# Performance work log

Hardware: AMD Instinct MI355X
Metric: run time of the kernel (lower is better)

The kernel has to match this reference:

```python
import jax, jax.numpy as jnp
import numpy as np

N_NODES = 100_000
N_EDGES = 1_600_000  # random edges; self-loops appended (add_self_edges_networkx)
IN_FEATS = 64
N_HIDDEN = 64
N_CLASSES = 40


def setup_inputs() -> dict:
    key = jax.random.key(0)
    ks = jax.random.split(key, 10)
    features = jax.random.normal(ks[0], (N_NODES, IN_FEATS), jnp.float32)
    self_loops = jnp.arange(N_NODES, dtype=jnp.int32)
    src = jnp.concatenate([jax.random.randint(ks[1], (N_EDGES,), 0, N_NODES, jnp.int32), self_loops])
    dst = jnp.concatenate([jax.random.randint(ks[2], (N_EDGES,), 0, N_NODES, jnp.int32), self_loops])
    labels = jax.random.randint(ks[3], (N_NODES,), 0, N_CLASSES, jnp.int32)
    mask = jnp.ones((N_NODES,), bool)
    s = 0.05
    W0 = jax.random.normal(ks[4], (IN_FEATS, N_HIDDEN), jnp.float32) * s
    b0 = jnp.zeros((N_HIDDEN,), jnp.float32)
    W1 = jax.random.normal(ks[5], (N_HIDDEN, N_HIDDEN), jnp.float32) * s
    b1 = jnp.zeros((N_HIDDEN,), jnp.float32)
    W2 = jax.random.normal(ks[6], (N_HIDDEN, N_CLASSES), jnp.float32) * s
    b2 = jnp.zeros((N_CLASSES,), jnp.float32)
    return {"features": features, "W0": W0, "b0": b0, "W1": W1, "b1": b1,
            "W2": W2, "b2": b2, "src": src, "dst": dst,
            "labels": labels, "mask": mask}


def reference(features, W0, b0, W1, b1, W2, b2, src, dst, labels, mask):
    # gcn_msg: pass src 'h'; gcn_reduce: sum over incoming messages;
    # NodeApplyModule: linear (+ activation on non-final layers).
    def gcn_layer(h, W, b, act):
        agg = jax.ops.segment_sum(h[src], dst, num_segments=N_NODES)  # gather -> sum reduce
        h = agg @ W + b
        return jax.nn.relu(h) if act else h

    h = gcn_layer(features, W0, b0, act=True)
    h = gcn_layer(h, W1, b1, act=True)
    rep = gcn_layer(h, W2, b2, act=False)  # [N, n_classes]

    # loss: fn_reduce=log_softmax over dim=0 (as written in the source), nll sum / count
    logp = jax.nn.log_softmax(rep, axis=0)
    picked = jnp.take_along_axis(logp, labels[:, None].astype(jnp.int32), axis=1)[:, 0]
    maskf = mask.astype(jnp.float32)
    loss = -jnp.sum(picked * maskf) / jnp.sum(maskf)
    return rep, loss
```

## Files before the change

kernel.cpp:

```cpp
#include <hip/hip_runtime.h>
#include <hip/hip_bf16.h>
#include <hip/hip_fp16.h>

#define NCLS 40

typedef __attribute__((ext_vector_type(8))) _Float16 half8;
typedef __attribute__((ext_vector_type(2))) _Float16 half2h;
union H2U { half2h h; unsigned u; };

#define EPB 16384
#define MAXB1 128
#define MAXNB 104

__global__ __launch_bounds__(256) void hist_and_gemm(
        const int* __restrict__ dst, int E, int nb, int* __restrict__ blockHist, int nB1,
        const float* __restrict__ X, const float* __restrict__ W,
        _Float16* __restrict__ out, int N) {
    __shared__ int cnt[4][MAXNB];
    int t = threadIdx.x;
    if ((int)blockIdx.x < nB1) {
        for (int i = t; i < 4 * MAXNB; i += 256) cnt[i / MAXNB][i % MAXNB] = 0;
        __syncthreads();
        int bk = t & 3;
        int base = blockIdx.x * EPB;
        int end = min(base + EPB, E);
        for (int i = base + t; i < end; i += 256) atomicAdd(&cnt[bk][dst[i] >> 10], 1);
        __syncthreads();
        for (int i = t; i < nb; i += 256)
            blockHist[blockIdx.x * nb + i] = cnt[0][i] + cnt[1][i] + cnt[2][i] + cnt[3][i];
        return;
    }
    int bid = blockIdx.x - nB1;
    int nBlocks = gridDim.x - nB1;
    int lane = t & 63;
    int waveId = (bid * 256 + t) >> 6;
    int nWaves = (nBlocks * 256) >> 6;
    int p = lane & 31;

    H2U wh[32];
#pragma unroll
    for (int j = 0; j < 32; ++j)
        wh[j].h = half2h{(_Float16)W[(2 * j) * 64 + lane], (_Float16)W[(2 * j + 1) * 64 + lane]};

    const float2* Xf = (const float2*)X;
    auto loadX = [&](int row) -> H2U {
        H2U r; r.u = 0;
        if (row < N) {
            float2 f = Xf[(size_t)row * 32 + p];
            r.h = half2h{(_Float16)f.x, (_Float16)f.y};
        }
        return r;
    };
    int row = waveId;
    H2U xp = loadX(row);
    for (; row < N; row += nWaves) {
        H2U nxt = loadX(row + nWaves);
        float y0 = 0.f, y1 = 0.f;
#pragma unroll
        for (int j2 = 0; j2 < 32; j2 += 2) {
            H2U r0, r1;
            r0.u = __builtin_amdgcn_readlane(xp.u, j2);
            r1.u = __builtin_amdgcn_readlane(xp.u, j2 + 1);
            y0 = __builtin_amdgcn_fdot2(r0.h, wh[j2].h, y0, false);
            y1 = __builtin_amdgcn_fdot2(r1.h, wh[j2 + 1].h, y1, false);
        }
        out[(size_t)row * 64 + lane] = (_Float16)(y0 + y1);
        xp = nxt;
    }
}

__global__ void bucket_scan(const int* __restrict__ blockHist, int nB1, int nb,
                            int* __restrict__ blockBase, int* __restrict__ bucketOffs,
                            int* __restrict__ offs, int N, int E, int* __restrict__ red32,
                            int* __restrict__ esrc) {
    __shared__ int h[MAXB1 * MAXNB];
    __shared__ int btot[MAXNB];
    __shared__ int boffs[MAXNB + 1];
    int t = threadIdx.x;
    if (t < 128) red32[t] = 0;
    int total = nB1 * nb;
    for (int i = t; i < total; i += 128) h[i] = blockHist[i];
    __syncthreads();
    for (int b = t; b < nb; b += 128) {
        int run = 0;
        for (int i = 0; i < nB1; ++i) { int v = h[i * nb + b]; h[i * nb + b] = run; run += v; }
        btot[b] = run;
    }
    __syncthreads();
    if (t == 0) {
        int run = 0;
        for (int b = 0; b < nb; ++b) { boffs[b] = run; run += btot[b]; }
        boffs[nb] = run;
    }
    __syncthreads();
    for (int b = t; b < nb; b += 128) {
        int bo = boffs[b];
        for (int i = 0; i < nB1; ++i) h[i * nb + b] += bo;
    }
    __syncthreads();
    for (int i = t; i < total; i += 128) blockBase[i] = h[i];
    for (int b = t; b <= nb; b += 128) bucketOffs[b] = boffs[b];
    if (t == 0) { offs[N] = E; }
    if (t < 8) esrc[E + t] = 0;
}

__global__ void bucket_place(const int* __restrict__ src, const int* __restrict__ dst, int E,
                             int nb, const int* __restrict__ blockBase,
                             unsigned* __restrict__ tmp) {
    __shared__ int cur[MAXNB];
    int t = threadIdx.x;
    for (int i = t; i < nb; i += 256) cur[i] = blockBase[blockIdx.x * nb + i];
    __syncthreads();
    int base = blockIdx.x * EPB;
    int end = min(base + EPB, E);
    for (int i = base + t; i < end; i += 256) {
        int d = dst[i];
        int s = src[i];
        unsigned pack = ((unsigned)(d & 1023) << 17) | (unsigned)s;
        int pos = atomicAdd(&cur[d >> 10], 1);
        tmp[pos] = pack;
    }
}

__global__ __launch_bounds__(512) void bucket_finalize(const unsigned* __restrict__ tmp,
                                                       const int* __restrict__ bucketOffs,
                                                       int N, int* __restrict__ offs,
                                                       int* __restrict__ esrc) {
    __shared__ int cnt[1024];
    __shared__ int wsum[8];
    int b = blockIdx.x;
    int t = threadIdx.x;
    int bstart = bucketOffs[b], bend = bucketOffs[b + 1];
    cnt[t] = 0;
    cnt[t + 512] = 0;
    __syncthreads();
    for (int i = bstart + t; i < bend; i += 512) atomicAdd(&cnt[tmp[i] >> 17], 1);
    __syncthreads();
    int c0 = cnt[2 * t], c1 = cnt[2 * t + 1];
    int s = c0 + c1;
    int lane = t & 63, w = t >> 6;
    int ssc = s;
    for (int off = 1; off < 64; off <<= 1) {
        int v = __shfl_up(ssc, off, 64);
        if (lane >= off) ssc += v;
    }
    if (lane == 63) wsum[w] = ssc;
    __syncthreads();
    int wo = 0;
#pragma unroll
    for (int k = 0; k < 8; ++k)
        if (k < w) wo += wsum[k];
    int excl = (ssc - s) + wo + bstart;
    __syncthreads();
    int node0 = (b << 10) + 2 * t;
    if (node0 < N) offs[node0] = excl;
    if (node0 + 1 < N) offs[node0 + 1] = excl + c0;
    cnt[2 * t] = excl;
    cnt[2 * t + 1] = excl + c0;
    __syncthreads();
    for (int i = bstart + t; i < bend; i += 512) {
        unsigned p = tmp[i];
        int pos = atomicAdd(&cnt[p >> 17], 1);
        esrc[pos] = (int)((((p >> 17) & 127u) << 17) | (p & 0x1FFFFu));
    }
}

__global__ __launch_bounds__(256) void gemm_fdot(const void* __restrict__ X, int xHalf,
                                                 const float* __restrict__ W,
                                                 const float* __restrict__ bias,
                                                 void* __restrict__ out, int outHalf,
                                                 int N, int FO) {
    int lane = threadIdx.x & 63;
    int waveId = (blockIdx.x * blockDim.x + threadIdx.x) >> 6;
    int nWaves = (gridDim.x * blockDim.x) >> 6;
    int cl = lane < FO ? lane : 0;
    int p = lane & 31;

    H2U wh[32];
#pragma unroll
    for (int j = 0; j < 32; ++j)
        wh[j].h = half2h{(_Float16)W[(2 * j) * FO + cl], (_Float16)W[(2 * j + 1) * FO + cl]};
    float gb = 0.f;
    if (bias != nullptr && lane < FO) gb = bias[lane];

    const unsigned* Xh = (const unsigned*)X;
    const float2* Xf = (const float2*)X;
    float* outF = (float*)out;
    _Float16* outH = (_Float16*)out;

    auto loadX = [&](int row) -> H2U {
        H2U r; r.u = 0;
        if (row < N) {
            if (xHalf) r.u = Xh[(size_t)row * 32 + p];
            else {
                float2 f = Xf[(size_t)row * 32 + p];
                r.h = half2h{(_Float16)f.x, (_Float16)f.y};
            }
        }
        return r;
    };

    int row = waveId;
    H2U xp = loadX(row);
    for (; row < N; row += nWaves) {
        H2U nxt = loadX(row + nWaves);
        float y0 = gb, y1 = 0.f;
#pragma unroll
        for (int j2 = 0; j2 < 32; j2 += 2) {
            H2U r0, r1;
            r0.u = __builtin_amdgcn_readlane(xp.u, j2);
            r1.u = __builtin_amdgcn_readlane(xp.u, j2 + 1);
            y0 = __builtin_amdgcn_fdot2(r0.h, wh[j2].h, y0, false);
            y1 = __builtin_amdgcn_fdot2(r1.h, wh[j2 + 1].h, y1, false);
        }
        float y = y0 + y1;
        if (lane < FO) {
            if (outHalf) outH[(size_t)row * FO + lane] = (_Float16)y;
            else         outF[(size_t)row * FO + lane] = y;
        }
        xp = nxt;
    }
}

#define ACC_PAIR(word, ae, ao)                                        \
    do {                                                              \
        H2U _p; _p.u = (word);                                        \
        (ae) = __builtin_amdgcn_fdot2(_p.h, selE.h, (ae), false);     \
        (ao) = __builtin_amdgcn_fdot2(_p.h, selO.h, (ao), false);     \
    } while (0)

#define GNODES 64
#define GSH 6
#define AST 66

template <int MODE>
__global__ __launch_bounds__(256) void agg_lds_kernel(
        const _Float16* __restrict__ t, const int* __restrict__ offs,
        const int* __restrict__ esrc, const float* __restrict__ bias,
        _Float16* __restrict__ out, int N) {
    __shared__ float acc[GNODES * AST];
    int tid = threadIdx.x;
    int g0 = blockIdx.x << GSH;
    int g1 = min(g0 + GNODES, N);
    for (int i = tid; i < GNODES * AST; i += 256) acc[i] = 0.f;
    int beg = offs[g0];
    int end = offs[g1];
    __syncthreads();

    int nE = end - beg;
    int chunk = (nE + 31) >> 5;
    int slot = tid >> 3;
    int oct = tid & 7;
    int e0 = beg + slot * chunk;
    int e1 = min(e0 + chunk, end);

    H2U selE, selO;
    selE.h = half2h{(_Float16)1.f, (_Float16)0.f};
    selO.h = half2h{(_Float16)0.f, (_Float16)1.f};

    float a[8];
#pragma unroll
    for (int k = 0; k < 8; ++k) a[k] = 0.f;

    if (e0 < e1) {
        int cur = -1;
        int pA = esrc[e0];
        int pB = esrc[e0 + 1];
        uint4 vA = *(const uint4*)(t + (size_t)(pA & 0x1FFFF) * 64 + oct * 8);
        for (int e = e0; e < e1; ++e) {
            int pC = esrc[e + 2];
            uint4 vB = *(const uint4*)(t + (size_t)(pB & 0x1FFFF) * 64 + oct * 8);
            int dl = (pA >> 17) & (GNODES - 1);
            if (dl != cur) {
                if (cur >= 0) {
                    float* fp = &acc[cur * AST + oct * 8];
#pragma unroll
                    for (int k = 0; k < 8; ++k) { atomicAdd(&fp[k], a[k]); a[k] = 0.f; }
                }
                cur = dl;
            }
            ACC_PAIR(vA.x, a[0], a[1]); ACC_PAIR(vA.y, a[2], a[3]);
            ACC_PAIR(vA.z, a[4], a[5]); ACC_PAIR(vA.w, a[6], a[7]);
            pA = pB; pB = pC; vA = vB;
        }
        float* fp = &acc[cur * AST + oct * 8];
#pragma unroll
        for (int k = 0; k < 8; ++k) atomicAdd(&fp[k], a[k]);
    }
    __syncthreads();

    for (int u = tid; u < GNODES * 8; u += 256) {
        int node = u >> 3, oc = u & 7;
        int gn = g0 + node;
        if (gn < N) {
            half8 hv;
#pragma unroll
            for (int k = 0; k < 8; ++k) {
                float v = acc[node * AST + oc * 8 + k];
                if (MODE == 0) v = fmaxf(v + bias[oc * 8 + k], 0.f);
                hv[k] = (_Float16)v;
            }
            *(half8*)(out + (size_t)gn * 64 + oc * 8) = hv;
        }
    }
}

__global__ void loss_pass(const float* __restrict__ rep, const int* __restrict__ labels, int N,
                          double* __restrict__ colSum, double* __restrict__ pickedSum,
                          int* __restrict__ cnt) {
    const int G = 8;
    const int ROWS = 512;
    int t = threadIdx.x;
    int c = t % NCLS;
    int g = t / NCLS;
    int base = blockIdx.x * ROWS;
    int lim = min(base + ROWS, N);
    double sumLoc = 0.0, pickLoc = 0.0;
    int cntLoc = 0;
    for (int r = base + g; r < lim; r += G) {
        float v = rep[(size_t)r * NCLS + c];
        sumLoc += exp((double)v);
        if (labels[r] == c) { pickLoc += (double)v; cntLoc++; }
    }
    __shared__ double colP[G][NCLS];
    __shared__ int cntP[G][NCLS];
    __shared__ double waveP[5];
    colP[g][c] = sumLoc;
    cntP[g][c] = cntLoc;
    __syncthreads();
    if (g == 0) {
        double tot = 0.0;
        int ctot = 0;
        for (int gg = 0; gg < G; ++gg) { tot += colP[gg][c]; ctot += cntP[gg][c]; }
        atomicAdd(&colSum[c], tot);
        if (ctot) atomicAdd(&cnt[c], ctot);
    }
    double wv = pickLoc;
    for (int off = 32; off; off >>= 1) wv += __shfl_down(wv, off, 64);
    if ((t & 63) == 0) waveP[t >> 6] = wv;
    __syncthreads();
    if (t == 0) {
        double s = 0.0;
        for (int i = 0; i < 5; ++i) s += waveP[i];
        atomicAdd(pickedSum, s);
    }
}

__global__ void finalize_kernel(const double* __restrict__ colSum, const int* __restrict__ cnt,
                                const double* __restrict__ pickedSum, int N,
                                float* __restrict__ lossOut) {
    int t = threadIdx.x;
    double term = 0.0;
    if (t < NCLS) term = (double)cnt[t] * log(colSum[t]);
    for (int off = 32; off; off >>= 1) term += __shfl_down(term, off, 64);
    if (t == 0) lossOut[0] = (float)((term - pickedSum[0]) / (double)N);
}

extern "C" void kernel_launch(void* const* d_in, const int* in_sizes, int n_in,
                              void* d_out, int out_size, void* d_ws, size_t ws_size,
                              hipStream_t stream) {
    const float* features = (const float*)d_in[0];
    const float* W0 = (const float*)d_in[1];
    const float* b0 = (const float*)d_in[2];
    const float* W1 = (const float*)d_in[3];
    const float* b1 = (const float*)d_in[4];
    const float* W2 = (const float*)d_in[5];
    const float* b2 = (const float*)d_in[6];
    const int* src = (const int*)d_in[7];
    const int* dst = (const int*)d_in[8];
    const int* labels = (const int*)d_in[9];

    const int N = in_sizes[0] / 64;
    const int E = in_sizes[7];
    const int NC = in_sizes[6];

    char* ws = (char*)d_ws;
    size_t off = 0;
    auto alloc = [&](size_t bytes) -> void* {
        void* p = ws + off;
        off = (off + bytes + 255) & ~(size_t)255;
        return p;
    };
    int* offs      = (int*)alloc((size_t)(N + 1) * 4);
    int* esrc      = (int*)alloc((size_t)(E + 8) * 4);
    _Float16* bufA = (_Float16*)alloc((size_t)N * 64 * 2);
    _Float16* bufB = (_Float16*)alloc((size_t)N * 64 * 2);
    unsigned* tmp  = (unsigned*)alloc((size_t)E * 4);
    int* blockHist = (int*)alloc((size_t)MAXB1 * MAXNB * 4);
    int* blockBase = (int*)alloc((size_t)MAXB1 * MAXNB * 4);
    int* bucketOffs= (int*)alloc((size_t)(MAXNB + 1) * 4);
    char* red      = (char*)alloc(512);
    double* colSum    = (double*)red;
    double* pickedSum = (double*)(red + 320);
    int* cntRed       = (int*)(red + 328);

    float* rep = (float*)d_out;
    float* lossOut = rep + (size_t)N * NC;

    const int nb  = (N + 1023) >> 10;
    const int nB1 = (E + EPB - 1) / EPB;

    hist_and_gemm<<<nB1 + 2048, 256, 0, stream>>>(dst, E, nb, blockHist, nB1,
                                                  features, W0, bufA, N);
    bucket_scan<<<1, 128, 0, stream>>>(blockHist, nB1, nb, blockBase, bucketOffs, offs, N, E,
                                       (int*)red, esrc);
    bucket_place<<<nB1, 256, 0, stream>>>(src, dst, E, nb, blockBase, tmp);
    bucket_finalize<<<nb, 512, 0, stream>>>(tmp, bucketOffs, N, offs, esrc);

    const int nGroups = (N + GNODES - 1) >> GSH;

    agg_lds_kernel<0><<<nGroups, 256, 0, stream>>>(bufA, offs, esrc, b0, bufB, N);
    gemm_fdot<<<2048, 256, 0, stream>>>(bufB, 1, W1, nullptr, bufA, 1, N, 64);
    agg_lds_kernel<0><<<nGroups, 256, 0, stream>>>(bufA, offs, esrc, b1, bufB, N);
    agg_lds_kernel<1><<<nGroups, 256, 0, stream>>>(bufB, offs, esrc, nullptr, bufA, N);
    gemm_fdot<<<2048, 256, 0, stream>>>(bufA, 1, W2, b2, rep, 0, N, NC);

    loss_pass<<<(N + 511) / 512, 320, 0, stream>>>(rep, labels, N, colSum, pickedSum, cntRed);
    finalize_kernel<<<1, 64, 0, stream>>>(colSum, cntRed, pickedSum, N, lossOut);
}
```

Baseline: 449.9 us.

## Split hidden features into column slabs and aggregate one node per wave

Hidden activations are stored as four column slabs of 16 halves per node, so each feature slab (3.2 MB) can stay cache-resident during the gather. The LDS-atomic group aggregation is replaced by a kernel that gives each wave one destination node and one slab, with 16 edge slots per wave and a shuffle reduction at the end, removing shared-memory atomics. Edge entries no longer pack a local destination id. This costs four times as many index reads, 8-byte gathers instead of 16-byte ones, and a large grid of small blocks with uneven per-node degree.

```diff
diff --git a/kernel.cpp b/kernel.cpp
--- a/kernel.cpp
+++ b/kernel.cpp
@@ -5,8 +5,10 @@
 #define NCLS 40
 
 typedef __attribute__((ext_vector_type(8))) _Float16 half8;
+typedef __attribute__((ext_vector_type(4))) _Float16 half4h;
 typedef __attribute__((ext_vector_type(2))) _Float16 half2h;
 union H2U { half2h h; unsigned u; };
+
 
 #define EPB 16384
 #define MAXB1 128
@@ -51,6 +53,7 @@
         }
         return r;
     };
+    int cg = lane >> 4, cc = lane & 15;
     int row = waveId;
     H2U xp = loadX(row);
     for (; row < N; row += nWaves) {
@@ -64,7 +67,7 @@
             y0 = __builtin_amdgcn_fdot2(r0.h, wh[j2].h, y0, false);
             y1 = __builtin_amdgcn_fdot2(r1.h, wh[j2 + 1].h, y1, false);
         }
-        out[(size_t)row * 64 + lane] = (_Float16)(y0 + y1);
+        out[((size_t)cg * N + row) * 16 + cc] = (_Float16)(y0 + y1);
         xp = nxt;
     }
 }
@@ -161,7 +164,7 @@
     for (int i = bstart + t; i < bend; i += 512) {
         unsigned p = tmp[i];
         int pos = atomicAdd(&cnt[p >> 17], 1);
-        esrc[pos] = (int)((((p >> 17) & 127u) << 17) | (p & 0x1FFFFu));
+        esrc[pos] = (int)(p & 0x1FFFFu);
     }
 }
 
@@ -187,11 +190,13 @@
     const float2* Xf = (const float2*)X;
     float* outF = (float*)out;
     _Float16* outH = (_Float16*)out;
+    int scg = p >> 3, su = p & 7;
+    int ocg = lane >> 4, occ = lane & 15;
 
     auto loadX = [&](int row) -> H2U {
         H2U r; r.u = 0;
         if (row < N) {
-            if (xHalf) r.u = Xh[(size_t)row * 32 + p];
+            if (xHalf) r.u = Xh[((size_t)scg * N + row) * 8 + su];
             else {
                 float2 f = Xf[(size_t)row * 32 + p];
                 r.h = half2h{(_Float16)f.x, (_Float16)f.y};
@@ -214,9 +219,10 @@
             y1 = __builtin_amdgcn_fdot2(r1.h, wh[j2 + 1].h, y1, false);
         }
         float y = y0 + y1;
-        if (lane < FO) {
-            if (outHalf) outH[(size_t)row * FO + lane] = (_Float16)y;
-            else         outF[(size_t)row * FO + lane] = y;
+        if (outHalf) {
+            outH[((size_t)ocg * N + row) * 16 + occ] = (_Float16)y;
+        } else if (lane < FO) {
+            outF[(size_t)row * FO + lane] = y;
         }
         xp = nxt;
     }
@@ -229,79 +235,58 @@
         (ao) = __builtin_amdgcn_fdot2(_p.h, selO.h, (ao), false);     \
     } while (0)
 
-#define GNODES 64
-#define GSH 6
-#define AST 66
-
 template <int MODE>
-__global__ __launch_bounds__(256) void agg_lds_kernel(
+__global__ __launch_bounds__(256) void agg_cs_kernel(
         const _Float16* __restrict__ t, const int* __restrict__ offs,
         const int* __restrict__ esrc, const float* __restrict__ bias,
         _Float16* __restrict__ out, int N) {
-    __shared__ float acc[GNODES * AST];
-    int tid = threadIdx.x;
-    int g0 = blockIdx.x << GSH;
-    int g1 = min(g0 + GNODES, N);
-    for (int i = tid; i < GNODES * AST; i += 256) acc[i] = 0.f;
-    int beg = offs[g0];
-    int end = offs[g1];
-    __syncthreads();
-
-    int nE = end - beg;
-    int chunk = (nE + 31) >> 5;
-    int slot = tid >> 3;
-    int oct = tid & 7;
-    int e0 = beg + slot * chunk;
-    int e1 = min(e0 + chunk, end);
+    int bid = blockIdx.x;
+    int cg = bid & 3;
+    int nb = bid >> 2;
+    int w = threadIdx.x >> 6;
+    int node = nb * 4 + w;
+    if (node >= N) return;
+    int lane = threadIdx.x & 63;
+    int sub = lane >> 2;
+    int l4 = lane & 3;
+    int beg = offs[node], end = offs[node + 1];
+    const _Float16* slab = t + (size_t)cg * N * 16;
 
     H2U selE, selO;
     selE.h = half2h{(_Float16)1.f, (_Float16)0.f};
     selO.h = half2h{(_Float16)0.f, (_Float16)1.f};
 
-    float a[8];
-#pragma unroll
-    for (int k = 0; k < 8; ++k) a[k] = 0.f;
-
-    if (e0 < e1) {
-        int cur = -1;
-        int pA = esrc[e0];
-        int pB = esrc[e0 + 1];
-        uint4 vA = *(const uint4*)(t + (size_t)(pA & 0x1FFFF) * 64 + oct * 8);
-        for (int e = e0; e < e1; ++e) {
-            int pC = esrc[e + 2];
-            uint4 vB = *(const uint4*)(t + (size_t)(pB & 0x1FFFF) * 64 + oct * 8);
-            int dl = (pA >> 17) & (GNODES - 1);
-            if (dl != cur) {
-                if (cur >= 0) {
-                    float* fp = &acc[cur * AST + oct * 8];
-#pragma unroll
-                    for (int k = 0; k < 8; ++k) { atomicAdd(&fp[k], a[k]); a[k] = 0.f; }
-                }
-                cur = dl;
-            }
-            ACC_PAIR(vA.x, a[0], a[1]); ACC_PAIR(vA.y, a[2], a[3]);
-            ACC_PAIR(vA.z, a[4], a[5]); ACC_PAIR(vA.w, a[6], a[7]);
-            pA = pB; pB = pC; vA = vB;
-        }
-        float* fp = &acc[cur * AST + oct * 8];
-#pragma unroll
-        for (int k = 0; k < 8; ++k) atomicAdd(&fp[k], a[k]);
-    }
-    __syncthreads();
-
-    for (int u = tid; u < GNODES * 8; u += 256) {
-        int node = u >> 3, oc = u & 7;
-        int gn = g0 + node;
-        if (gn < N) {
-            half8 hv;
-#pragma unroll
-            for (int k = 0; k < 8; ++k) {
-                float v = acc[node * AST + oc * 8 + k];
-                if (MODE == 0) v = fmaxf(v + bias[oc * 8 + k], 0.f);
-                hv[k] = (_Float16)v;
-            }
-            *(half8*)(out + (size_t)gn * 64 + oc * 8) = hv;
-        }
+    float a[4] = {0.f, 0.f, 0.f, 0.f};
+    int j = beg + sub;
+    if (j < end) {
+        int s = esrc[j];
+        uint2 v = *(const uint2*)(slab + (size_t)s * 16 + l4 * 4);
+        for (j += 16; j < end; j += 16) {
+            int sn = esrc[j];
+            uint2 vn = *(const uint2*)(slab + (size_t)sn * 16 + l4 * 4);
+            ACC_PAIR(v.x, a[0], a[1]);
+            ACC_PAIR(v.y, a[2], a[3]);
+            v = vn;
+        }
+        ACC_PAIR(v.x, a[0], a[1]);
+        ACC_PAIR(v.y, a[2], a[3]);
+    }
+#pragma unroll
+    for (int k = 0; k < 4; ++k) {
+        a[k] += __shfl_xor(a[k], 4, 64);
+        a[k] += __shfl_xor(a[k], 8, 64);
+        a[k] += __shfl_xor(a[k], 16, 64);
+        a[k] += __shfl_xor(a[k], 32, 64);
+    }
+    if (sub == 0) {
+        half4h hv;
+#pragma unroll
+        for (int k = 0; k < 4; ++k) {
+            float vv = a[k];
+            if (MODE == 0) vv = fmaxf(vv + bias[cg * 16 + l4 * 4 + k], 0.f);
+            hv[k] = (_Float16)vv;
+        }
+        *(half4h*)(out + ((size_t)cg * N + node) * 16 + l4 * 4) = hv;
     }
 }
 
@@ -407,12 +392,13 @@
     bucket_place<<<nB1, 256, 0, stream>>>(src, dst, E, nb, blockBase, tmp);
     bucket_finalize<<<nb, 512, 0, stream>>>(tmp, bucketOffs, N, offs, esrc);
 
-    const int nGroups = (N + GNODES - 1) >> GSH;
-
-    agg_lds_kernel<0><<<nGroups, 256, 0, stream>>>(bufA, offs, esrc, b0, bufB, N);
+    const int nbNode = (N + 3) >> 2;
+    const int aggGrid = nbNode * 4;
+
+    agg_cs_kernel<0><<<aggGrid, 256, 0, stream>>>(bufA, offs, esrc, b0, bufB, N);
     gemm_fdot<<<2048, 256, 0, stream>>>(bufB, 1, W1, nullptr, bufA, 1, N, 64);
-    agg_lds_kernel<0><<<nGroups, 256, 0, stream>>>(bufA, offs, esrc, b1, bufB, N);
-    agg_lds_kernel<1><<<nGroups, 256, 0, stream>>>(bufB, offs, esrc, nullptr, bufA, N);
+    agg_cs_kernel<0><<<aggGrid, 256, 0, stream>>>(bufA, offs, esrc, b1, bufB, N);
+    agg_cs_kernel<1><<<aggGrid, 256, 0, stream>>>(bufB, offs, esrc, nullptr, bufA, N);
     gemm_fdot<<<2048, 256, 0, stream>>>(bufA, 1, W2, b2, rep, 0, N, NC);
 
     loss_pass<<<(N + 511) / 512, 320, 0, stream>>>(rep, labels, N, colSum, pickedSum, cntRed);
```

Result: slower. 549.3 us (+22.1%).
